# Kernel optimization log

Measured on AMD Instinct MI355X. Metric: run time of the kernel, lower is better.

Reference implementation:

```python
import jax, jax.numpy as jnp
import numpy as np

# dims: batch, seq(tokens, excl cls), input_dim, embed_dim, heads, ffn, experts, proto experts, classes
B, S, DIN, D, H, FF, E, P, NC = 2, 2048, 1024, 512, 8, 2048, 6, 4, 2
CAP = int(1.0 * S / E)  # capacity_factor=1.0


def _ln(x, g, b, eps=1e-5):
    m = x.mean(-1, keepdims=True)
    v = ((x - m) ** 2).mean(-1, keepdims=True)
    return (x - m) / jnp.sqrt(v + eps) * g + b


def _gelu(x):
    return jax.nn.gelu(x, approximate=False)


def _mha(x, in_w, in_b, out_w, out_b):
    # torch nn.MultiheadAttention, batch_first, eval (no dropout)
    b, s, d = x.shape
    dh = d // H
    qkv = x @ in_w.T + in_b
    q, k, v = jnp.split(qkv, 3, axis=-1)
    q = q.reshape(b, s, H, dh)
    k = k.reshape(b, s, H, dh)
    v = v.reshape(b, s, H, dh)
    att = jnp.einsum('bqhd,bkhd->bhqk', q, k) * (1.0 / np.sqrt(dh))
    att = jax.nn.softmax(att, axis=-1)
    o = jnp.einsum('bhqk,bkhd->bqhd', att, v).reshape(b, s, d)
    return o @ out_w.T + out_b


def _subln_ffn(x, w1, b1, lg, lb, w2, b2):
    # FeedForwardNetwork with subln: fc1 -> gelu -> LayerNorm -> fc2 (eval: no dropout)
    h = _gelu(x @ w1 + b1)
    h = _ln(h, lg, lb)
    return h @ w2 + b2


def _pamoe(x, gate_w, W1, b1, W2, b2):
    # top-1 prototype-augmented MoE with capacity-based token drop
    gate = jax.nn.softmax(x @ gate_w, axis=-1)          # [B,S,E]
    idx = jnp.argmax(gate, axis=-1)                      # [B,S]
    top_p = jnp.max(gate, axis=-1)                       # [B,S]
    oh = jax.nn.one_hot(idx, E, dtype=x.dtype)           # [B,S,E]
    pos = jnp.cumsum(oh, axis=1) * oh                    # position within expert
    keep = oh * (pos <= CAP)                             # capacity mask
    out = jnp.zeros_like(x)
    for e in range(E):  # small fixed loop over experts
        m = (keep[..., e] * top_p)[..., None]
        out = out + m * (_gelu(x @ W1[e] + b1[e]) @ W2[e] + b2[e])
    return out, gate


def _pamoe_ce(gate, labels):
    # CE between renormalized prototype-expert gate probs and cosine-sim labels
    p = gate[..., :P]
    logp = jnp.log(p / p.sum(-1, keepdims=True) + 1e-9)
    nll = -jnp.take_along_axis(logp, labels[..., None], axis=-1)[..., 0]
    return nll.mean()


def setup_inputs() -> dict:
    key = jax.random.key(0)
    cnt = [0]
    def nk():
        cnt[0] += 1
        return jax.random.fold_in(key, cnt[0])
    def w(*shape):
        return jax.random.normal(nk(), shape, dtype=jnp.float32) * 0.02
    d = {}
    d['x'] = jax.random.normal(nk(), (B, S, DIN), dtype=jnp.float32)
    d['protos'] = jax.random.normal(nk(), (P, DIN), dtype=jnp.float32)
    d['cls_token'] = jax.random.normal(nk(), (1, 1, D), dtype=jnp.float32)
    d['fc1_w'] = w(DIN, D); d['fc1_b'] = jnp.zeros((D,), jnp.float32)
    for li in ('l0', 'l1'):
        d[li + '_attn_in_w'] = w(3 * D, D); d[li + '_attn_in_b'] = jnp.zeros((3 * D,), jnp.float32)
        d[li + '_attn_out_w'] = w(D, D); d[li + '_attn_out_b'] = jnp.zeros((D,), jnp.float32)
        d[li + '_n1_g'] = jnp.ones((D,), jnp.float32); d[li + '_n1_b'] = jnp.zeros((D,), jnp.float32)
        d[li + '_n2_g'] = jnp.ones((D,), jnp.float32); d[li + '_n2_b'] = jnp.zeros((D,), jnp.float32)
    # layer0: pamoe + cls_ffn
    d['l0_cls_w1'] = w(D, FF); d['l0_cls_b1'] = jnp.zeros((FF,), jnp.float32)
    d['l0_cls_ln_g'] = jnp.ones((FF,), jnp.float32); d['l0_cls_ln_b'] = jnp.zeros((FF,), jnp.float32)
    d['l0_cls_w2'] = w(FF, D); d['l0_cls_b2'] = jnp.zeros((D,), jnp.float32)
    d['l0_gate_w'] = w(D, E)
    d['l0_e_w1'] = w(E, D, FF); d['l0_e_b1'] = jnp.zeros((E, FF), jnp.float32)
    d['l0_e_w2'] = w(E, FF, D); d['l0_e_b2'] = jnp.zeros((E, D), jnp.float32)
    # layer1: dense ffn
    d['l1_ffn_w1'] = w(D, FF); d['l1_ffn_b1'] = jnp.zeros((FF,), jnp.float32)
    d['l1_ffn_ln_g'] = jnp.ones((FF,), jnp.float32); d['l1_ffn_ln_b'] = jnp.zeros((FF,), jnp.float32)
    d['l1_ffn_w2'] = w(FF, D); d['l1_ffn_b2'] = jnp.zeros((D,), jnp.float32)
    d['norm_g'] = jnp.ones((D,), jnp.float32); d['norm_b'] = jnp.zeros((D,), jnp.float32)
    d['fc2_w'] = w(D, NC); d['fc2_b'] = jnp.zeros((NC,), jnp.float32)
    return d


def reference(x, protos, cls_token, fc1_w, fc1_b,
              l0_attn_in_w, l0_attn_in_b, l0_attn_out_w, l0_attn_out_b,
              l0_n1_g, l0_n1_b, l0_n2_g, l0_n2_b,
              l0_cls_w1, l0_cls_b1, l0_cls_ln_g, l0_cls_ln_b, l0_cls_w2, l0_cls_b2,
              l0_gate_w, l0_e_w1, l0_e_b1, l0_e_w2, l0_e_b2,
              l1_attn_in_w, l1_attn_in_b, l1_attn_out_w, l1_attn_out_b,
              l1_n1_g, l1_n1_b, l1_n2_g, l1_n2_b,
              l1_ffn_w1, l1_ffn_b1, l1_ffn_ln_g, l1_ffn_ln_b, l1_ffn_w2, l1_ffn_b2,
              norm_g, norm_b, fc2_w, fc2_b):
    # prototype cosine similarity on raw (detached) features -> routing supervision labels
    xr = jax.lax.stop_gradient(x)
    xn = xr / (jnp.linalg.norm(xr, axis=-1, keepdims=True) + 1e-8)
    pn = protos / (jnp.linalg.norm(protos, axis=-1, keepdims=True) + 1e-8)
    sim = jnp.einsum('bsd,pd->bsp', xn, pn)             # [B,S,P]
    labels = jnp.argmax(sim, axis=-1)                    # [B,S]

    h = x @ fc1_w + fc1_b                                # [B,S,D]
    cls = jnp.broadcast_to(cls_token, (h.shape[0], 1, D))
    h = jnp.concatenate([cls, h], axis=1)                # [B,S+1,D]

    # ---- layer 0 (pamoe block) ----
    attn = _mha(h, l0_attn_in_w, l0_attn_in_b, l0_attn_out_w, l0_attn_out_b)
    h = _ln(h, l0_n1_g, l0_n1_b)
    h = h + attn
    h = _ln(h, l0_n2_g, l0_n2_b)
    h_res = h
    c = _subln_ffn(h[:, 0:1], l0_cls_w1, l0_cls_b1, l0_cls_ln_g, l0_cls_ln_b, l0_cls_w2, l0_cls_b2)
    t, gate = _pamoe(h[:, 1:], l0_gate_w, l0_e_w1, l0_e_b1, l0_e_w2, l0_e_b2)
    h = h_res + jnp.concatenate([c, t], axis=1)          # pamoe residual
    loss_pamoe = _pamoe_ce(gate, labels)

    # ---- layer 1 (dense ffn block) ----
    attn = _mha(h, l1_attn_in_w, l1_attn_in_b, l1_attn_out_w, l1_attn_out_b)
    h = _ln(h, l1_n1_g, l1_n1_b)
    h = h + attn
    h = _ln(h, l1_n2_g, l1_n2_b)
    h = h + _subln_ffn(h, l1_ffn_w1, l1_ffn_b1, l1_ffn_ln_g, l1_ffn_ln_b, l1_ffn_w2, l1_ffn_b2)

    pooled = _ln(h, norm_g, norm_b)[:, 0]                # cls token
    logits = pooled @ fc2_w + fc2_b                      # [B,NC]
    return gate, logits, loss_pamoe
```

## Files before the change

kernel.cpp:

```cpp
#include <hip/hip_runtime.h>
#include <cmath>

#define DEVINL __device__ __forceinline__

typedef unsigned short ushort_t;
typedef unsigned int uint_t;

constexpr int Bb   = 2;
constexpr int Ss   = 2048;
constexpr int S1   = 2049;
constexpr int DIN  = 1024;
constexpr int Dd   = 512;
constexpr int Hh   = 8;
constexpr int FF   = 2048;
constexpr int Ee   = 6;
constexpr int NCc  = 2;
constexpr int CAP  = 341;
constexpr int NTOK = Bb * Ss;
constexpr int RR   = Bb * S1;
constexpr int MOE_ROWS = Bb * CAP;

typedef __attribute__((ext_vector_type(4))) float f32x4;
typedef __attribute__((ext_vector_type(8))) short bf16x8;

DEVINL float geluf(float x) { return 0.5f * x * (1.0f + erff(x * 0.7071067811865476f)); }

DEVINL ushort_t f2bf(float f) {
  uint_t u = __float_as_uint(f);
  u += 0x7FFFu + ((u >> 16) & 1u);
  return (ushort_t)(u >> 16);
}
DEVINL float bf2f(ushort_t u) { return __uint_as_float((uint_t)u << 16); }

DEVINL void glds16(const ushort_t* g, void* lds) {
  __builtin_amdgcn_global_load_lds(
      (const __attribute__((address_space(1))) void*)g,
      (__attribute__((address_space(3))) void*)lds, 16, 0, 0);
}

DEVINL float wsum(float v) {
#pragma unroll
  for (int off = 32; off; off >>= 1) v += __shfl_xor(v, off);
  return v;
}
DEVINL float bsum(float v, float* red) {
  v = wsum(v);
  int w = threadIdx.x >> 6;
  if ((threadIdx.x & 63) == 0) red[w] = v;
  __syncthreads();
  float r = red[0] + red[1] + red[2] + red[3];
  __syncthreads();
  return r;
}

constexpr int C5_N0 = NTOK * DIN / 8;
constexpr int C5_N1 = 3 * Dd * Dd / 8;
constexpr int C5_N2 = Dd * Dd / 8;
constexpr int C5_T  = C5_N0 + 2 * C5_N1 + 2 * C5_N2;
__global__ __launch_bounds__(256) void cast5_kernel(const float* __restrict__ s0, ushort_t* __restrict__ d0,
                                                    const float* __restrict__ s1, ushort_t* __restrict__ d1,
                                                    const float* __restrict__ s2, ushort_t* __restrict__ d2,
                                                    const float* __restrict__ s3, ushort_t* __restrict__ d3,
                                                    const float* __restrict__ s4, ushort_t* __restrict__ d4) {
  int i = blockIdx.x * 256 + threadIdx.x;
  if (i >= C5_T) return;
  const float* src; ushort_t* dst; int off;
  if (i < C5_N0) { src = s0; dst = d0; off = i; }
  else if (i < C5_N0 + C5_N1) { src = s1; dst = d1; off = i - C5_N0; }
  else if (i < C5_N0 + C5_N1 + C5_N2) { src = s2; dst = d2; off = i - C5_N0 - C5_N1; }
  else if (i < C5_N0 + 2 * C5_N1 + C5_N2) { src = s3; dst = d3; off = i - C5_N0 - C5_N1 - C5_N2; }
  else { src = s4; dst = d4; off = i - C5_N0 - 2 * C5_N1 - C5_N2; }
  float4 a = *(const float4*)(src + (size_t)off * 8);
  float4 b = *(const float4*)(src + (size_t)off * 8 + 4);
  bf16x8 v;
  v[0] = (short)f2bf(a.x); v[1] = (short)f2bf(a.y);
  v[2] = (short)f2bf(a.z); v[3] = (short)f2bf(a.w);
  v[4] = (short)f2bf(b.x); v[5] = (short)f2bf(b.y);
  v[6] = (short)f2bf(b.z); v[7] = (short)f2bf(b.w);
  *(bf16x8*)(dst + (size_t)off * 8) = v;
}

__global__ __launch_bounds__(256) void tpose_cast_kernel(const float* __restrict__ in,
                                                         ushort_t* __restrict__ outp,
                                                         int K, int N) {
  __shared__ float t[64][65];
  const int z = blockIdx.z;
  const float* src = in + (size_t)z * K * N;
  ushort_t* dst = outp + (size_t)z * K * N;
  const int k0 = blockIdx.x * 64, n0 = blockIdx.y * 64;
  const int tx = threadIdx.x & 15, ty = threadIdx.x >> 4;
#pragma unroll
  for (int p = 0; p < 4; ++p) {
    int k = ty + p * 16;
    float4 v = *(const float4*)(src + (size_t)(k0 + k) * N + n0 + tx * 4);
    t[k][tx * 4 + 0] = v.x; t[k][tx * 4 + 1] = v.y;
    t[k][tx * 4 + 2] = v.z; t[k][tx * 4 + 3] = v.w;
  }
  __syncthreads();
#pragma unroll
  for (int p = 0; p < 4; ++p) {
    int n = ty + p * 16;
    uint_t lo = (uint_t)f2bf(t[tx * 4 + 0][n]) | ((uint_t)f2bf(t[tx * 4 + 1][n]) << 16);
    uint_t hi = (uint_t)f2bf(t[tx * 4 + 2][n]) | ((uint_t)f2bf(t[tx * 4 + 3][n]) << 16);
    *(uint2*)(dst + (size_t)(n0 + n) * K + k0 + tx * 4) = make_uint2(lo, hi);
  }
}

__global__ __launch_bounds__(256) void labels_kernel(const float* __restrict__ x,
                                                     const float* __restrict__ protos,
                                                     int* __restrict__ lbl) {
  int t = blockIdx.x * 4 + (threadIdx.x >> 6);
  int lane = threadIdx.x & 63;
  if (t >= NTOK) return;
  const float* xr = x + (size_t)t * DIN;
  float xv[16];
  float ss = 0.f;
#pragma unroll
  for (int i = 0; i < 16; ++i) { xv[i] = xr[lane + 64 * i]; ss += xv[i] * xv[i]; }
  ss = wsum(ss);
  float nx = sqrtf(ss) + 1e-8f;
  float best = -2e30f; int bi = 0;
  for (int p = 0; p < 4; ++p) {
    const float* pr = protos + (size_t)p * DIN;
    float dp = 0.f, pp = 0.f;
#pragma unroll
    for (int i = 0; i < 16; ++i) { float v = pr[lane + 64 * i]; dp += v * xv[i]; pp += v * v; }
    dp = wsum(dp); pp = wsum(pp);
    float sim = dp / (nx * (sqrtf(pp) + 1e-8f));
    if (sim > best) { best = sim; bi = p; }
  }
  if (lane == 0) lbl[t] = bi;
}

template <bool ACT, bool SHIFT, int BMT>
__global__ __launch_bounds__(256) void mgemm_kernel(const ushort_t* __restrict__ A, int lda,
                                                    const ushort_t* __restrict__ Bw, int ldb,
                                                    const float* __restrict__ bias,
                                                    const ushort_t* __restrict__ res,
                                                    ushort_t* __restrict__ C, int ldc,
                                                    int M, int N, int K) {
  constexpr int MI = BMT / 32;
  __shared__ ushort_t As[BMT * 64];
  __shared__ ushort_t Bs[128 * 64];
  const int tid = threadIdx.x;
  const int l = tid & 63, l15 = l & 15, lg = l >> 4;
  const int w = tid >> 6;
  const int wm = w >> 1, wn = w & 1;
  const int bm = blockIdx.x * BMT, bn = blockIdx.y * 128;
  const int srowA = w * (BMT / 4) + (l >> 3);
  const int srowB = w * 32 + (l >> 3);
  const int scc = ((l & 7) ^ (l >> 3)) * 8;

  f32x4 acc[MI][4];
#pragma unroll
  for (int i = 0; i < MI; ++i)
#pragma unroll
    for (int j = 0; j < 4; ++j) acc[i][j] = (f32x4){0.f, 0.f, 0.f, 0.f};

  const ushort_t* agp[MI];
  const ushort_t* bgp[4];
#pragma unroll
  for (int j = 0; j < MI; ++j) {
    int ar = bm + srowA + j * 8; if (ar > M - 1) ar = M - 1;
    agp[j] = A + (size_t)ar * lda + scc;
  }
#pragma unroll
  for (int j = 0; j < 4; ++j)
    bgp[j] = Bw + (size_t)(bn + srowB + j * 8) * ldb + scc;

  for (int k0 = 0; k0 < K; k0 += 64) {
#pragma unroll
    for (int j = 0; j < MI; ++j)
      glds16(agp[j] + k0, (char*)As + w * (BMT * 32) + j * 1024);
#pragma unroll
    for (int j = 0; j < 4; ++j)
      glds16(bgp[j] + k0, (char*)Bs + w * 4096 + j * 1024);
    __syncthreads();
#pragma unroll
    for (int kc = 0; kc < 2; ++kc) {
      bf16x8 af[MI], bfr[4];
#pragma unroll
      for (int mi = 0; mi < MI; ++mi) {
        int row = wm * (BMT / 2) + mi * 16 + l15;
        af[mi] = *(const bf16x8*)((const char*)As +
                   ((row * 128 + (kc * 32 + lg * 8) * 2) ^ ((row & 7) << 4)));
      }
#pragma unroll
      for (int ni = 0; ni < 4; ++ni) {
        int row = wn * 64 + ni * 16 + l15;
        bfr[ni] = *(const bf16x8*)((const char*)Bs +
                   ((row * 128 + (kc * 32 + lg * 8) * 2) ^ ((row & 7) << 4)));
      }
#pragma unroll
      for (int mi = 0; mi < MI; ++mi)
#pragma unroll
        for (int ni = 0; ni < 4; ++ni)
          acc[mi][ni] = __builtin_amdgcn_mfma_f32_16x16x32_bf16(af[mi], bfr[ni], acc[mi][ni], 0, 0, 0);
    }
    __syncthreads();
  }

#pragma unroll
  for (int mi = 0; mi < MI; ++mi)
#pragma unroll
    for (int r = 0; r < 4; ++r) {
      int row = bm + wm * (BMT / 2) + mi * 16 + lg * 4 + r;
      if (row < M) {
        int orow = SHIFT ? (row + (row >> 11) + 1) : row;
#pragma unroll
        for (int ni = 0; ni < 4; ++ni) {
          int col = bn + wn * 64 + ni * 16 + l15;
          float t = acc[mi][ni][r];
          if (bias) t += bias[col];
          if (ACT) t = geluf(t);
          if (res) t += bf2f(res[(size_t)orow * ldc + col]);
          C[(size_t)orow * ldc + col] = f2bf(t);
        }
      }
    }
}

__global__ __launch_bounds__(256) void moe_mgemm1_kernel(const ushort_t* __restrict__ h2,
                                                         const ushort_t* __restrict__ w1T,
                                                         const float* __restrict__ b1all,
                                                         const int* __restrict__ list,
                                                         const int* __restrict__ cnt,
                                                         ushort_t* __restrict__ hid) {
  __shared__ ushort_t As[128 * 64];
  __shared__ ushort_t Bs[128 * 64];
  const int e = blockIdx.z;
  const int c0 = cnt[e * 2 + 0], c1 = cnt[e * 2 + 1];
  const ushort_t* Bw = w1T + (size_t)e * Dd * FF;
  const int tid = threadIdx.x;
  const int l = tid & 63, l15 = l & 15, lg = l >> 4;
  const int w = tid >> 6;
  const int wm = w >> 1, wn = w & 1;
  const int bm = blockIdx.x * 128, bn = blockIdx.y * 128;
  const int srow = w * 32 + (l >> 3);
  const int scc = ((l & 7) ^ (l >> 3)) * 8;

  f32x4 acc[4][4];
#pragma unroll
  for (int i = 0; i < 4; ++i)
#pragma unroll
    for (int j = 0; j < 4; ++j) acc[i][j] = (f32x4){0.f, 0.f, 0.f, 0.f};

  const ushort_t* agp[4];
  const ushort_t* bgp[4];
#pragma unroll
  for (int j = 0; j < 4; ++j) {
    int r = bm + srow + j * 8; if (r > MOE_ROWS - 1) r = MOE_ROWS - 1;
    int tok = list[e * MOE_ROWS + r] & (NTOK - 1);
    int b = tok >> 11, s = tok & (Ss - 1);
    agp[j] = h2 + (size_t)(b * S1 + s + 1) * Dd + scc;
    bgp[j] = Bw + (size_t)(bn + srow + j * 8) * Dd + scc;
  }

  for (int k0 = 0; k0 < Dd; k0 += 64) {
#pragma unroll
    for (int j = 0; j < 4; ++j) {
      glds16(agp[j] + k0, (char*)As + w * 4096 + j * 1024);
      glds16(bgp[j] + k0, (char*)Bs + w * 4096 + j * 1024);
    }
    __syncthreads();
#pragma unroll
    for (int kc = 0; kc < 2; ++kc) {
      bf16x8 af[4], bfr[4];
#pragma unroll
      for (int mi = 0; mi < 4; ++mi) {
        int row = wm * 64 + mi * 16 + l15;
        af[mi] = *(const bf16x8*)((const char*)As +
                   ((row * 128 + (kc * 32 + lg * 8) * 2) ^ ((row & 7) << 4)));
      }
#pragma unroll
      for (int ni = 0; ni < 4; ++ni) {
        int row = wn * 64 + ni * 16 + l15;
        bfr[ni] = *(const bf16x8*)((const char*)Bs +
                   ((row * 128 + (kc * 32 + lg * 8) * 2) ^ ((row & 7) << 4)));
      }
#pragma unroll
      for (int mi = 0; mi < 4; ++mi)
#pragma unroll
        for (int ni = 0; ni < 4; ++ni)
          acc[mi][ni] = __builtin_amdgcn_mfma_f32_16x16x32_bf16(af[mi], bfr[ni], acc[mi][ni], 0, 0, 0);
    }
    __syncthreads();
  }

#pragma unroll
  for (int mi = 0; mi < 4; ++mi)
#pragma unroll
    for (int rr = 0; rr < 4; ++rr) {
      int row = bm + wm * 64 + mi * 16 + lg * 4 + rr;
      bool v2 = (row < MOE_ROWS) && ((row < CAP) ? (row < c0) : ((row - CAP) < c1));
      if (v2) {
#pragma unroll
        for (int ni = 0; ni < 4; ++ni) {
          int col = bn + wn * 64 + ni * 16 + l15;
          hid[((size_t)e * MOE_ROWS + row) * FF + col] =
              f2bf(geluf(acc[mi][ni][rr] + b1all[e * FF + col]));
        }
      }
    }
}

template <int BMT>
__global__ __launch_bounds__(256) void moe_mgemm2_kernel(const ushort_t* __restrict__ hid,
                                                         const ushort_t* __restrict__ w2T,
                                                         const float* __restrict__ b2all,
                                                         const int* __restrict__ list,
                                                         const int* __restrict__ cnt,
                                                         const float* __restrict__ topp,
                                                         ushort_t* __restrict__ out) {
  constexpr int MI = BMT / 32;
  __shared__ ushort_t As[BMT * 64];
  __shared__ ushort_t Bs[128 * 64];
  const int e = blockIdx.z;
  const int c0 = cnt[e * 2 + 0], c1 = cnt[e * 2 + 1];
  const ushort_t* Bw = w2T + (size_t)e * FF * Dd;
  const int tid = threadIdx.x;
  const int l = tid & 63, l15 = l & 15, lg = l >> 4;
  const int w = tid >> 6;
  const int wm = w >> 1, wn = w & 1;
  const int bm = blockIdx.x * BMT, bn = blockIdx.y * 128;
  const int srowA = w * (BMT / 4) + (l >> 3);
  const int srowB = w * 32 + (l >> 3);
  const int scc = ((l & 7) ^ (l >> 3)) * 8;

  f32x4 acc[MI][4];
#pragma unroll
  for (int i = 0; i < MI; ++i)
#pragma unroll
    for (int j = 0; j < 4; ++j) acc[i][j] = (f32x4){0.f, 0.f, 0.f, 0.f};

  const ushort_t* agp[MI];
  const ushort_t* bgp[4];
#pragma unroll
  for (int j = 0; j < MI; ++j) {
    int r = bm + srowA + j * 8; if (r > MOE_ROWS - 1) r = MOE_ROWS - 1;
    agp[j] = hid + ((size_t)e * MOE_ROWS + r) * FF + scc;
  }
#pragma unroll
  for (int j = 0; j < 4; ++j)
    bgp[j] = Bw + (size_t)(bn + srowB + j * 8) * FF + scc;

  for (int k0 = 0; k0 < FF; k0 += 64) {
#pragma unroll
    for (int j = 0; j < MI; ++j)
      glds16(agp[j] + k0, (char*)As + w * (BMT * 32) + j * 1024);
#pragma unroll
    for (int j = 0; j < 4; ++j)
      glds16(bgp[j] + k0, (char*)Bs + w * 4096 + j * 1024);
    __syncthreads();
#pragma unroll
    for (int kc = 0; kc < 2; ++kc) {
      bf16x8 af[MI], bfr[4];
#pragma unroll
      for (int mi = 0; mi < MI; ++mi) {
        int row = wm * (BMT / 2) + mi * 16 + l15;
        af[mi] = *(const bf16x8*)((const char*)As +
                   ((row * 128 + (kc * 32 + lg * 8) * 2) ^ ((row & 7) << 4)));
      }
#pragma unroll
      for (int ni = 0; ni < 4; ++ni) {
        int row = wn * 64 + ni * 16 + l15;
        bfr[ni] = *(const bf16x8*)((const char*)Bs +
                   ((row * 128 + (kc * 32 + lg * 8) * 2) ^ ((row & 7) << 4)));
      }
#pragma unroll
      for (int mi = 0; mi < MI; ++mi)
#pragma unroll
        for (int ni = 0; ni < 4; ++ni)
          acc[mi][ni] = __builtin_amdgcn_mfma_f32_16x16x32_bf16(af[mi], bfr[ni], acc[mi][ni], 0, 0, 0);
    }
    __syncthreads();
  }

#pragma unroll
  for (int mi = 0; mi < MI; ++mi)
#pragma unroll
    for (int rr = 0; rr < 4; ++rr) {
      int row = bm + wm * (BMT / 2) + mi * 16 + lg * 4 + rr;
      bool v2 = (row < MOE_ROWS) && ((row < CAP) ? (row < c0) : ((row - CAP) < c1));
      if (v2) {
        int tok = list[e * MOE_ROWS + row];
        int b = tok >> 11, s = tok & (Ss - 1);
        float tp = topp[tok];
#pragma unroll
        for (int ni = 0; ni < 4; ++ni) {
          int col = bn + wn * 64 + ni * 16 + l15;
          size_t oidx = (size_t)(b * S1 + s + 1) * Dd + col;
          out[oidx] = f2bf(bf2f(out[oidx]) + tp * (acc[mi][ni][rr] + b2all[e * Dd + col]));
        }
      }
    }
}

__global__ __launch_bounds__(256) void cls_fill_kernel(const float* __restrict__ cls,
                                                       ushort_t* __restrict__ h) {
  int i = threadIdx.x;
  uint_t pk = (uint_t)f2bf(cls[i * 2]) | ((uint_t)f2bf(cls[i * 2 + 1]) << 16);
  *(uint_t*)(h + i * 2) = pk;
  *(uint_t*)(h + (size_t)S1 * Dd + i * 2) = pk;
}

template <int EPL>
__global__ __launch_bounds__(256) void ln_wave_kernel(const ushort_t* __restrict__ in,
                                                      const ushort_t* __restrict__ addv,
                                                      const float* __restrict__ g,
                                                      const float* __restrict__ bvec,
                                                      ushort_t* __restrict__ out,
                                                      ushort_t* __restrict__ out2,
                                                      int nrows) {
  constexpr int N = 64 * EPL;
  const int row = blockIdx.x * 4 + (threadIdx.x >> 6);
  const int lane = threadIdx.x & 63;
  if (row >= nrows) return;
  const size_t base = (size_t)row * N + lane * EPL;
  float xf[EPL];
  float s1 = 0.f, s2 = 0.f;
#pragma unroll
  for (int c = 0; c < EPL / 8; ++c) {
    bf16x8 x8 = *(const bf16x8*)(in + base + c * 8);
#pragma unroll
    for (int j = 0; j < 8; ++j) {
      float v = bf2f((ushort_t)x8[j]);
      xf[c * 8 + j] = v;
      s1 += v; s2 += v * v;
    }
  }
  s1 = wsum(s1); s2 = wsum(s2);
  float mean = s1 * (1.0f / N);
  float var = s2 * (1.0f / N) - mean * mean;
  float rstd = rsqrtf(var + 1e-5f);
#pragma unroll
  for (int c = 0; c < EPL / 8; ++c) {
    bf16x8 a8;
    if (addv) a8 = *(const bf16x8*)(addv + base + c * 8);
    bf16x8 o8;
#pragma unroll
    for (int j = 0; j < 8; ++j) {
      int col = lane * EPL + c * 8 + j;
      float v = (xf[c * 8 + j] - mean) * rstd * g[col] + bvec[col];
      if (addv) v += bf2f((ushort_t)a8[j]);
      o8[j] = (short)f2bf(v);
    }
    *(bf16x8*)(out + base + c * 8) = o8;
    if (out2) *(bf16x8*)(out2 + base + c * 8) = o8;
  }
}

__global__ __launch_bounds__(256) void ln2_wave_kernel(const ushort_t* __restrict__ in,
                                                       const ushort_t* __restrict__ addv,
                                                       const float* __restrict__ g1,
                                                       const float* __restrict__ b1,
                                                       const float* __restrict__ g2,
                                                       const float* __restrict__ b2,
                                                       ushort_t* __restrict__ out,
                                                       ushort_t* __restrict__ out2,
                                                       int nrows) {
  constexpr int N = 512;
  const int row = blockIdx.x * 4 + (threadIdx.x >> 6);
  const int lane = threadIdx.x & 63;
  if (row >= nrows) return;
  const size_t base = (size_t)row * N + lane * 8;
  bf16x8 x8 = *(const bf16x8*)(in + base);
  bf16x8 a8 = *(const bf16x8*)(addv + base);
  float xf[8];
  float s1 = 0.f, s2 = 0.f;
#pragma unroll
  for (int j = 0; j < 8; ++j) {
    float v = bf2f((ushort_t)x8[j]);
    xf[j] = v; s1 += v; s2 += v * v;
  }
  s1 = wsum(s1); s2 = wsum(s2);
  float mean = s1 * (1.0f / N);
  float rstd = rsqrtf(s2 * (1.0f / N) - mean * mean + 1e-5f);
  float vf[8];
  float t1 = 0.f, t2 = 0.f;
#pragma unroll
  for (int j = 0; j < 8; ++j) {
    int col = lane * 8 + j;
    float v = (xf[j] - mean) * rstd * g1[col] + b1[col] + bf2f((ushort_t)a8[j]);
    vf[j] = v; t1 += v; t2 += v * v;
  }
  t1 = wsum(t1); t2 = wsum(t2);
  float mean2 = t1 * (1.0f / N);
  float rstd2 = rsqrtf(t2 * (1.0f / N) - mean2 * mean2 + 1e-5f);
  bf16x8 o8;
#pragma unroll
  for (int j = 0; j < 8; ++j) {
    int col = lane * 8 + j;
    o8[j] = (short)f2bf((vf[j] - mean2) * rstd2 * g2[col] + b2[col]);
  }
  *(bf16x8*)(out + base) = o8;
  if (out2) *(bf16x8*)(out2 + base) = o8;
}

__global__ __launch_bounds__(256) void attn_mfma_kernel(const ushort_t* __restrict__ qkv,
                                                        ushort_t* __restrict__ o) {
  __shared__ ushort_t Ksh[128 * 64];
  __shared__ ushort_t Vt[64 * 128];
  const int tid = threadIdx.x;
  const int w = tid >> 6, l = tid & 63;
  const int l15 = l & 15, lg = l >> 4;
  const int hh = blockIdx.y, b = blockIdx.z;
  const int qblk = blockIdx.x * 64;
  const size_t rbase = (size_t)b * S1 * 1536;
  const float CEXP = 0.125f * 1.4426950408889634f;

  bf16x8 aq[2];
  {
    int qr = qblk + w * 16 + l15;
    const ushort_t* qp = qkv + rbase + (size_t)qr * 1536 + hh * 64;
#pragma unroll
    for (int dc = 0; dc < 2; ++dc)
      aq[dc] = (qr < S1) ? *(const bf16x8*)(qp + dc * 32 + lg * 8)
                         : (bf16x8){0, 0, 0, 0, 0, 0, 0, 0};
  }

  f32x4 ovac[4];
#pragma unroll
  for (int dt = 0; dt < 4; ++dt) ovac[dt] = (f32x4){0.f, 0.f, 0.f, 0.f};
  float m_r = -1e30f, l_r = 0.f;

  const int kcc = ((l & 7) ^ (l >> 3)) * 8;
  const int krloc = w * 32 + (l >> 3);
  const int sv_k0 = (tid & 63) * 2, sv_d0 = (tid >> 6) * 16;

  for (int it = 0; it < 17; ++it) {
    {
      int rb = it * 128 + krloc;
#pragma unroll
      for (int pass = 0; pass < 4; ++pass) {
        int key = rb + pass * 8;
        if (key > S1 - 1) key = S1 - 1;
        glds16(qkv + rbase + (size_t)key * 1536 + 512 + hh * 64 + kcc,
               (char*)Ksh + w * 4096 + pass * 1024);
      }
    }
    {
      int key0 = it * 128 + sv_k0;
      int k0c = (key0 > S1 - 1) ? S1 - 1 : key0;
      int k1c = (key0 + 1 > S1 - 1) ? S1 - 1 : key0 + 1;
      const ushort_t* vp0 = qkv + rbase + (size_t)k0c * 1536 + 1024 + hh * 64 + sv_d0;
      const ushort_t* vp1 = qkv + rbase + (size_t)k1c * 1536 + 1024 + hh * 64 + sv_d0;
      bf16x8 va0 = *(const bf16x8*)(vp0), va1 = *(const bf16x8*)(vp0 + 8);
      bf16x8 vb0 = *(const bf16x8*)(vp1), vb1 = *(const bf16x8*)(vp1 + 8);
#pragma unroll
      for (int i = 0; i < 8; ++i) {
        int d0 = sv_d0 + i, d1 = sv_d0 + 8 + i;
        uint_t p0 = (uint_t)(ushort_t)va0[i] | ((uint_t)(ushort_t)vb0[i] << 16);
        uint_t p1 = (uint_t)(ushort_t)va1[i] | ((uint_t)(ushort_t)vb1[i] << 16);
        *(uint_t*)((char*)Vt + ((d0 * 256 + sv_k0 * 2) ^ ((d0 & 7) << 4))) = p0;
        *(uint_t*)((char*)Vt + ((d1 * 256 + sv_k0 * 2) ^ ((d1 & 7) << 4))) = p1;
      }
    }
    __syncthreads();

    f32x4 s[8];
    __builtin_amdgcn_s_setprio(1);
#pragma unroll
    for (int kt = 0; kt < 8; ++kt) {
      f32x4 acc = (f32x4){0.f, 0.f, 0.f, 0.f};
      const int krow = kt * 16 + l15;
      const int rswz = (krow & 7) << 4;
#pragma unroll
      for (int dc = 0; dc < 2; ++dc) {
        bf16x8 kb = *(const bf16x8*)((const char*)Ksh + (((krow * 64 + dc * 32 + lg * 8) * 2) ^ rswz));
        acc = __builtin_amdgcn_mfma_f32_16x16x32_bf16(kb, aq[dc], acc, 0, 0, 0);
      }
      s[kt] = acc;
    }
    __builtin_amdgcn_s_setprio(0);
    if (it == 16) {
#pragma unroll
      for (int kt = 0; kt < 8; ++kt)
#pragma unroll
        for (int r = 0; r < 4; ++r)
          if (2048 + kt * 16 + lg * 4 + r >= S1) s[kt][r] = -1e30f;
    }

    f32x4 m4 = s[0];
#pragma unroll
    for (int kt = 1; kt < 8; ++kt)
#pragma unroll
      for (int r = 0; r < 4; ++r) m4[r] = fmaxf(m4[r], s[kt][r]);
    float mx = fmaxf(fmaxf(m4[0], m4[1]), fmaxf(m4[2], m4[3]));
    mx = fmaxf(mx, __shfl_xor(mx, 16));
    mx = fmaxf(mx, __shfl_xor(mx, 32));
    if (!__all(mx <= m_r + 8.0f)) {
      float mn = fmaxf(m_r, mx);
      float fac = __builtin_amdgcn_exp2f((m_r - mn) * CEXP);
      m_r = mn;
      float facq[4];
#pragma unroll
      for (int r = 0; r < 4; ++r) facq[r] = __shfl(fac, lg * 4 + r);
#pragma unroll
      for (int dt = 0; dt < 4; ++dt)
#pragma unroll
        for (int r = 0; r < 4; ++r) ovac[dt][r] *= facq[r];
      l_r *= fac;
    }
    float mc = m_r * CEXP;
    float rs = 0.f;
#pragma unroll
    for (int kt = 0; kt < 8; ++kt)
#pragma unroll
      for (int r = 0; r < 4; ++r) {
        float pv = __builtin_amdgcn_exp2f(s[kt][r] * CEXP - mc);
        s[kt][r] = pv;
        rs += pv;
      }
    rs += __shfl_xor(rs, 16);
    rs += __shfl_xor(rs, 32);
    l_r += rs;

    uint_t pk[8][2];
#pragma unroll
    for (int kt = 0; kt < 8; ++kt) {
      pk[kt][0] = (uint_t)f2bf(s[kt][0]) | ((uint_t)f2bf(s[kt][1]) << 16);
      pk[kt][1] = (uint_t)f2bf(s[kt][2]) | ((uint_t)f2bf(s[kt][3]) << 16);
    }

    bf16x8 pa[4];
#pragma unroll
    for (int kh = 0; kh < 4; ++kh) {
      union { uint_t u[4]; bf16x8 v; } cu;
#pragma unroll
      for (int wd = 0; wd < 4; ++wd) {
        int src = (((2 * lg + (wd >> 1)) & 3) << 4) + l15;
        uint_t c0 = (uint_t)__shfl((int)pk[kh * 2 + 0][wd & 1], src);
        uint_t c1 = (uint_t)__shfl((int)pk[kh * 2 + 1][wd & 1], src);
        cu.u[wd] = (lg & 2) ? c1 : c0;
      }
      pa[kh] = cu.v;
    }

    __builtin_amdgcn_s_setprio(1);
#pragma unroll
    for (int kh = 0; kh < 4; ++kh)
#pragma unroll
      for (int dt = 0; dt < 4; ++dt) {
        const int vrow = dt * 16 + l15;
        bf16x8 vb = *(const bf16x8*)((const char*)Vt +
                      (((vrow * 256 + (kh * 32 + lg * 8) * 2)) ^ ((vrow & 7) << 4)));
        ovac[dt] = __builtin_amdgcn_mfma_f32_16x16x32_bf16(pa[kh], vb, ovac[dt], 0, 0, 0);
      }
    __builtin_amdgcn_s_setprio(0);
    __syncthreads();
  }

  float invq[4];
#pragma unroll
  for (int r = 0; r < 4; ++r) invq[r] = 1.0f / __shfl(l_r, lg * 4 + r);
#pragma unroll
  for (int r = 0; r < 4; ++r) {
    int qq = qblk + w * 16 + lg * 4 + r;
    if (qq < S1) {
      ushort_t* orow = o + (size_t)(b * S1 + qq) * Dd + hh * 64;
#pragma unroll
      for (int dt = 0; dt < 4; ++dt) orow[dt * 16 + l15] = f2bf(ovac[dt][r] * invq[r]);
    }
  }
}

__global__ __launch_bounds__(256) void gate_kernel(const ushort_t* __restrict__ h2,
                                                   const float* __restrict__ gw,
                                                   float* __restrict__ gate_out,
                                                   float* __restrict__ topp,
                                                   int* __restrict__ idx) {
  int t = blockIdx.x * 4 + (threadIdx.x >> 6);
  int lane = threadIdx.x & 63;
  if (t >= NTOK) return;
  int b = t >> 11, s = t & (Ss - 1);
  const ushort_t* hr = h2 + (size_t)(b * S1 + s + 1) * Dd;
  bf16x8 h8 = *(const bf16x8*)(hr + lane * 8);
  float acc[6] = {};
#pragma unroll
  for (int j = 0; j < 8; ++j) {
    int d = lane * 8 + j;
    float xv = bf2f((ushort_t)h8[j]);
    const float* g = gw + (size_t)d * Ee;
#pragma unroll
    for (int e = 0; e < 6; ++e) acc[e] += xv * g[e];
  }
#pragma unroll
  for (int e = 0; e < 6; ++e) acc[e] = wsum(acc[e]);
  if (lane == 0) {
    float mx = acc[0];
#pragma unroll
    for (int e = 1; e < 6; ++e) mx = fmaxf(mx, acc[e]);
    float ex[6], sum = 0.f;
#pragma unroll
    for (int e = 0; e < 6; ++e) { ex[e] = __expf(acc[e] - mx); sum += ex[e]; }
    float invs = 1.0f / sum;
    int best = 0; float bp = ex[0];
#pragma unroll
    for (int e = 1; e < 6; ++e) { if (ex[e] > bp) { bp = ex[e]; best = e; } }
#pragma unroll
    for (int e = 0; e < 6; ++e) gate_out[(size_t)t * Ee + e] = ex[e] * invs;
    topp[t] = bp * invs;
    idx[t] = best;
  }
}

__global__ __launch_bounds__(256) void route_kernel(const int* __restrict__ idx,
                                                    int* __restrict__ list,
                                                    int* __restrict__ cnt) {
  __shared__ int cnts[256];
  __shared__ int tot;
  const int e = blockIdx.x, b = blockIdx.y;
  const int tid = threadIdx.x;
  const int s0 = tid * 8;
  int loc[8];
  int c = 0;
#pragma unroll
  for (int j = 0; j < 8; ++j) {
    int t = b * Ss + s0 + j;
    if (idx[t] == e) loc[c++] = t;
  }
  cnts[tid] = c;
  __syncthreads();
  if (tid == 0) {
    int run = 0;
    for (int i = 0; i < 256; ++i) { int v = cnts[i]; cnts[i] = run; run += v; }
    tot = run;
  }
  __syncthreads();
  int base = cnts[tid];
  for (int j = 0; j < c; ++j) {
    int pos = base + j;
    if (pos < CAP) list[e * MOE_ROWS + b * CAP + pos] = loc[j];
  }
  if (tid == 0) cnt[e * Bb + b] = (tot < CAP) ? tot : CAP;
}

__global__ __launch_bounds__(256) void cls_ffn1_kernel(const ushort_t* __restrict__ h2,
                                                       const float* __restrict__ w1,
                                                       const float* __restrict__ b1,
                                                       float* __restrict__ chid) {
  __shared__ float hrow[Dd];
  __shared__ float red[8][32];
  const int b = blockIdx.y, tid = threadIdx.x;
  const int cl = tid & 31, kp = tid >> 5;
  const int col = blockIdx.x * 32 + cl;
  const ushort_t* hr = h2 + (size_t)(b * S1) * Dd;
  hrow[tid] = bf2f(hr[tid]);
  hrow[tid + 256] = bf2f(hr[tid + 256]);
  __syncthreads();
  float acc = 0.f;
#pragma unroll 8
  for (int j = 0; j < 64; ++j) {
    int d = kp * 64 + j;
    acc += hrow[d] * w1[(size_t)d * FF + col];
  }
  red[kp][cl] = acc;
  __syncthreads();
  if (kp == 0) {
    float s = b1[col];
#pragma unroll
    for (int i = 0; i < 8; ++i) s += red[i][cl];
    chid[b * FF + col] = geluf(s);
  }
}

__global__ __launch_bounds__(256) void cls_ln_kernel(const float* __restrict__ chid,
                                                     const float* __restrict__ lg,
                                                     const float* __restrict__ lb,
                                                     float* __restrict__ chln) {
  __shared__ float red[8];
  const int b = blockIdx.x, tid = threadIdx.x;
  const float* hr = chid + b * FF;
  float hv[8];
  float s1 = 0.f, s2 = 0.f;
#pragma unroll
  for (int j = 0; j < 8; ++j) {
    hv[j] = hr[tid + j * 256];
    s1 += hv[j]; s2 += hv[j] * hv[j];
  }
  s1 = bsum(s1, red);
  s2 = bsum(s2, red);
  float mean = s1 * (1.0f / FF);
  float rstd = rsqrtf(s2 * (1.0f / FF) - mean * mean + 1e-5f);
#pragma unroll
  for (int j = 0; j < 8; ++j) {
    int k = tid + j * 256;
    chln[b * FF + k] = (hv[j] - mean) * rstd * lg[k] + lb[k];
  }
}

__global__ __launch_bounds__(256) void cls_ffn2_kernel(const float* __restrict__ chln,
                                                       const float* __restrict__ w2,
                                                       const float* __restrict__ b2,
                                                       ushort_t* __restrict__ outbuf) {
  __shared__ float red[8][32];
  const int b = blockIdx.y, tid = threadIdx.x;
  const int cl = tid & 31, kp = tid >> 5;
  const int col = blockIdx.x * 32 + cl;
  const float* hr = chln + b * FF;
  float acc = 0.f;
#pragma unroll 8
  for (int j = 0; j < 256; ++j) {
    int k = kp * 256 + j;
    acc += hr[k] * w2[(size_t)k * Dd + col];
  }
  red[kp][cl] = acc;
  __syncthreads();
  if (kp == 0) {
    float s = b2[col];
#pragma unroll
    for (int i = 0; i < 8; ++i) s += red[i][cl];
    size_t oidx = (size_t)(b * S1) * Dd + col;
    outbuf[oidx] = f2bf(bf2f(outbuf[oidx]) + s);
  }
}

__global__ __launch_bounds__(256) void loss_part_kernel(const float* __restrict__ gate,
                                                        const int* __restrict__ lbl,
                                                        float* __restrict__ part) {
  __shared__ float red[8];
  int t = blockIdx.x * 256 + threadIdx.x;
  float v = 0.f;
  if (t < NTOK) {
    const float* p = gate + (size_t)t * Ee;
    float sum = p[0] + p[1] + p[2] + p[3];
    float pl = p[lbl[t]];
    v = -logf(pl / sum + 1e-9f);
  }
  v = bsum(v, red);
  if (threadIdx.x == 0) part[blockIdx.x] = v;
}

__global__ void loss_final_kernel(const float* __restrict__ part, float* __restrict__ out) {
  if (threadIdx.x == 0) {
    float s = 0.f;
    for (int i = 0; i < 16; ++i) s += part[i];
    out[NTOK * Ee + Bb * NCc] = s / (float)NTOK;
  }
}

__global__ __launch_bounds__(256) void final_head_kernel(const ushort_t* __restrict__ h,
                                                         const float* __restrict__ g,
                                                         const float* __restrict__ bvec,
                                                         const float* __restrict__ w,
                                                         const float* __restrict__ fb,
                                                         float* __restrict__ out) {
  __shared__ float red[8];
  int b = blockIdx.x, tid = threadIdx.x;
  const ushort_t* hr = h + (size_t)(b * S1) * Dd;
  float x0 = bf2f(hr[tid]), x1 = bf2f(hr[tid + 256]);
  float s1 = bsum(x0 + x1, red);
  float s2 = bsum(x0 * x0 + x1 * x1, red);
  float mean = s1 * (1.0f / Dd);
  float var = s2 * (1.0f / Dd) - mean * mean;
  float rstd = rsqrtf(var + 1e-5f);
  float p0 = (x0 - mean) * rstd * g[tid] + bvec[tid];
  float p1 = (x1 - mean) * rstd * g[tid + 256] + bvec[tid + 256];
  float l0 = p0 * w[tid * 2 + 0] + p1 * w[(tid + 256) * 2 + 0];
  float l1 = p0 * w[tid * 2 + 1] + p1 * w[(tid + 256) * 2 + 1];
  l0 = bsum(l0, red);
  l1 = bsum(l1, red);
  if (tid == 0) {
    out[NTOK * Ee + b * NCc + 0] = l0 + fb[0];
    out[NTOK * Ee + b * NCc + 1] = l1 + fb[1];
  }
}

extern "C" void kernel_launch(void* const* d_in, const int* in_sizes, int n_in,
                              void* d_out, int out_size, void* d_ws, size_t ws_size,
                              hipStream_t stream) {
  (void)in_sizes; (void)n_in; (void)out_size; (void)ws_size;
  const float* x       = (const float*)d_in[0];
  const float* protos  = (const float*)d_in[1];
  const float* cls_tok = (const float*)d_in[2];
  const float* fc1_w   = (const float*)d_in[3];
  const float* fc1_b   = (const float*)d_in[4];
  const float* a0_in_w = (const float*)d_in[5];
  const float* a0_in_b = (const float*)d_in[6];
  const float* a0_out_w= (const float*)d_in[7];
  const float* a0_out_b= (const float*)d_in[8];
  const float* n1g0    = (const float*)d_in[9];
  const float* n1b0    = (const float*)d_in[10];
  const float* n2g0    = (const float*)d_in[11];
  const float* n2b0    = (const float*)d_in[12];
  const float* a1_in_w = (const float*)d_in[13];
  const float* a1_in_b = (const float*)d_in[14];
  const float* a1_out_w= (const float*)d_in[15];
  const float* a1_out_b= (const float*)d_in[16];
  const float* n1g1    = (const float*)d_in[17];
  const float* n1b1    = (const float*)d_in[18];
  const float* n2g1    = (const float*)d_in[19];
  const float* n2b1    = (const float*)d_in[20];
  const float* cw1     = (const float*)d_in[21];
  const float* cb1     = (const float*)d_in[22];
  const float* clg     = (const float*)d_in[23];
  const float* clb     = (const float*)d_in[24];
  const float* cw2     = (const float*)d_in[25];
  const float* cb2     = (const float*)d_in[26];
  const float* gate_w  = (const float*)d_in[27];
  const float* ew1     = (const float*)d_in[28];
  const float* eb1     = (const float*)d_in[29];
  const float* ew2     = (const float*)d_in[30];
  const float* eb2     = (const float*)d_in[31];
  const float* fw1     = (const float*)d_in[32];
  const float* fb1     = (const float*)d_in[33];
  const float* flg     = (const float*)d_in[34];
  const float* flb     = (const float*)d_in[35];
  const float* fw2     = (const float*)d_in[36];
  const float* fb2     = (const float*)d_in[37];
  const float* ng      = (const float*)d_in[38];
  const float* nb      = (const float*)d_in[39];
  const float* fc2_w   = (const float*)d_in[40];
  const float* fc2_b   = (const float*)d_in[41];
  float* out = (float*)d_out;

  char* base = (char*)d_ws;
  size_t o = 0;
  auto alloc = [&](size_t bytes) -> void* {
    void* p = base + o;
    o += (bytes + 255) & ~(size_t)255;
    return p;
  };
  ushort_t* UB0  = (ushort_t*)alloc((size_t)RR * Dd * 2);
  ushort_t* UB1  = (ushort_t*)alloc((size_t)RR * Dd * 2);
  ushort_t* UB2  = (ushort_t*)alloc((size_t)RR * Dd * 2);
  ushort_t* BIGU = (ushort_t*)alloc((size_t)RR * FF * 2);
  ushort_t* XB   = (ushort_t*)alloc((size_t)NTOK * DIN * 2);
  ushort_t* WQ0  = (ushort_t*)alloc((size_t)3 * Dd * Dd * 2);
  ushort_t* WO0  = (ushort_t*)alloc((size_t)Dd * Dd * 2);
  ushort_t* WQ1  = (ushort_t*)alloc((size_t)3 * Dd * Dd * 2);
  ushort_t* WO1  = (ushort_t*)alloc((size_t)Dd * Dd * 2);
  ushort_t* WF1T = (ushort_t*)alloc((size_t)Dd * DIN * 2);
  ushort_t* WE1T = (ushort_t*)alloc((size_t)Ee * FF * Dd * 2);
  ushort_t* WE2T = (ushort_t*)alloc((size_t)Ee * Dd * FF * 2);
  ushort_t* WFW1T= (ushort_t*)alloc((size_t)FF * Dd * 2);
  ushort_t* WFW2T= (ushort_t*)alloc((size_t)Dd * FF * 2);
  float* TOPP = (float*)alloc(NTOK * 4);
  float* PART = (float*)alloc(64 * 4);
  float* CHID = (float*)alloc(Bb * FF * 4);
  float* CHLN = (float*)alloc(Bb * FF * 4);
  int* LBL  = (int*)alloc(NTOK * 4);
  int* IDX  = (int*)alloc(NTOK * 4);
  int* LIST = (int*)alloc(Ee * MOE_ROWS * 4);
  int* CNT  = (int*)alloc(Ee * Bb * 4);

  const int ln_grid = (RR + 3) / 4;

  cast5_kernel<<<(C5_T + 255) / 256, 256, 0, stream>>>(
      x, XB, a0_in_w, WQ0, a0_out_w, WO0, a1_in_w, WQ1, a1_out_w, WO1);
  tpose_cast_kernel<<<dim3(DIN / 64, Dd / 64, 1), 256, 0, stream>>>(fc1_w, WF1T, DIN, Dd);
  tpose_cast_kernel<<<dim3(Dd / 64, FF / 64, Ee), 256, 0, stream>>>(ew1, WE1T, Dd, FF);
  tpose_cast_kernel<<<dim3(FF / 64, Dd / 64, Ee), 256, 0, stream>>>(ew2, WE2T, FF, Dd);
  tpose_cast_kernel<<<dim3(Dd / 64, FF / 64, 1), 256, 0, stream>>>(fw1, WFW1T, Dd, FF);
  tpose_cast_kernel<<<dim3(FF / 64, Dd / 64, 1), 256, 0, stream>>>(fw2, WFW2T, FF, Dd);

  labels_kernel<<<NTOK / 4, 256, 0, stream>>>(x, protos, LBL);
  mgemm_kernel<false, true, 64><<<dim3(64, 4), 256, 0, stream>>>(
      XB, DIN, WF1T, DIN, fc1_b, nullptr, UB0, Dd, NTOK, Dd, DIN);
  cls_fill_kernel<<<1, 256, 0, stream>>>(cls_tok, UB0);

  mgemm_kernel<false, false, 64><<<dim3(65, 12), 256, 0, stream>>>(
      UB0, Dd, WQ0, Dd, a0_in_b, nullptr, BIGU, 3 * Dd, RR, 3 * Dd, Dd);
  attn_mfma_kernel<<<dim3(33, Hh, Bb), 256, 0, stream>>>(BIGU, UB1);
  mgemm_kernel<false, false, 64><<<dim3(65, 4), 256, 0, stream>>>(
      UB1, Dd, WO0, Dd, a0_out_b, nullptr, UB2, Dd, RR, Dd, Dd);
  ln2_wave_kernel<<<ln_grid, 256, 0, stream>>>(UB0, UB2, n1g0, n1b0, n2g0, n2b0, UB0, UB2, RR);

  cls_ffn1_kernel<<<dim3(FF / 32, Bb), 256, 0, stream>>>(UB0, cw1, cb1, CHID);
  cls_ln_kernel<<<Bb, 256, 0, stream>>>(CHID, clg, clb, CHLN);
  cls_ffn2_kernel<<<dim3(Dd / 32, Bb), 256, 0, stream>>>(CHLN, cw2, cb2, UB2);
  gate_kernel<<<NTOK / 4, 256, 0, stream>>>(UB0, gate_w, out, TOPP, IDX);
  route_kernel<<<dim3(Ee, Bb), 256, 0, stream>>>(IDX, LIST, CNT);
  moe_mgemm1_kernel<<<dim3(6, 16, Ee), 256, 0, stream>>>(UB0, WE1T, eb1, LIST, CNT, BIGU);
  moe_mgemm2_kernel<64><<<dim3(11, 4, Ee), 256, 0, stream>>>(BIGU, WE2T, eb2, LIST, CNT, TOPP, UB2);
  loss_part_kernel<<<16, 256, 0, stream>>>(out, LBL, PART);
  loss_final_kernel<<<1, 64, 0, stream>>>(PART, out);

  mgemm_kernel<false, false, 64><<<dim3(65, 12), 256, 0, stream>>>(
      UB2, Dd, WQ1, Dd, a1_in_b, nullptr, BIGU, 3 * Dd, RR, 3 * Dd, Dd);
  attn_mfma_kernel<<<dim3(33, Hh, Bb), 256, 0, stream>>>(BIGU, UB1);
  mgemm_kernel<false, false, 64><<<dim3(65, 4), 256, 0, stream>>>(
      UB1, Dd, WO1, Dd, a1_out_b, nullptr, UB0, Dd, RR, Dd, Dd);
  ln2_wave_kernel<<<ln_grid, 256, 0, stream>>>(UB2, UB0, n1g1, n1b1, n2g1, n2b1, UB2, nullptr, RR);

  mgemm_kernel<true, false, 128><<<dim3(33, 16), 256, 0, stream>>>(
      UB2, Dd, WFW1T, Dd, fb1, nullptr, BIGU, FF, RR, FF, Dd);
  ln_wave_kernel<32><<<ln_grid, 256, 0, stream>>>(BIGU, nullptr, flg, flb, BIGU, nullptr, RR);
  mgemm_kernel<false, false, 64><<<dim3(65, 4), 256, 0, stream>>>(
      BIGU, FF, WFW2T, FF, fb2, UB2, UB0, Dd, RR, Dd, FF);

  final_head_kernel<<<Bb, 256, 0, stream>>>(UB0, ng, nb, fc2_w, fc2_b, out);
}
```

Measured before the change: 491.2 us.

## Double-buffer attention K/V loads, shrink MoE and FFN1 GEMM row tiles

The attention kernel now double-buffers the K tile in shared memory and prefetches the next block's V into registers while the current block computes. V is written transposed into a padded, re-swizzled layout after the compute step, which removes the load-then-sync stall at the top of each iteration. Separately, the MoE first GEMM is templated on row tile size and launched with 64-row tiles, and the dense FFN1 GEMM also switches to 64-row tiles. Both launch more blocks to fill the GPU better, at the cost of more weight reloads and extra LDS use and syncs in attention.

New measurement: 507.8 us. 1.03x slower.

```diff
diff --git a/kernel.cpp b/kernel.cpp
--- a/kernel.cpp
+++ b/kernel.cpp
@@ -220,13 +220,15 @@
     }
 }
 
+template <int BMT>
 __global__ __launch_bounds__(256) void moe_mgemm1_kernel(const ushort_t* __restrict__ h2,
                                                          const ushort_t* __restrict__ w1T,
                                                          const float* __restrict__ b1all,
                                                          const int* __restrict__ list,
                                                          const int* __restrict__ cnt,
                                                          ushort_t* __restrict__ hid) {
-  __shared__ ushort_t As[128 * 64];
+  constexpr int MI = BMT / 32;
+  __shared__ ushort_t As[BMT * 64];
   __shared__ ushort_t Bs[128 * 64];
   const int e = blockIdx.z;
   const int c0 = cnt[e * 2 + 0], c1 = cnt[e * 2 + 1];
@@ -235,40 +237,44 @@
   const int l = tid & 63, l15 = l & 15, lg = l >> 4;
   const int w = tid >> 6;
   const int wm = w >> 1, wn = w & 1;
-  const int bm = blockIdx.x * 128, bn = blockIdx.y * 128;
-  const int srow = w * 32 + (l >> 3);
+  const int bm = blockIdx.x * BMT, bn = blockIdx.y * 128;
+  const int srowA = w * (BMT / 4) + (l >> 3);
+  const int srowB = w * 32 + (l >> 3);
   const int scc = ((l & 7) ^ (l >> 3)) * 8;
 
-  f32x4 acc[4][4];
-#pragma unroll
-  for (int i = 0; i < 4; ++i)
+  f32x4 acc[MI][4];
+#pragma unroll
+  for (int i = 0; i < MI; ++i)
 #pragma unroll
     for (int j = 0; j < 4; ++j) acc[i][j] = (f32x4){0.f, 0.f, 0.f, 0.f};
 
-  const ushort_t* agp[4];
+  const ushort_t* agp[MI];
   const ushort_t* bgp[4];
 #pragma unroll
-  for (int j = 0; j < 4; ++j) {
-    int r = bm + srow + j * 8; if (r > MOE_ROWS - 1) r = MOE_ROWS - 1;
+  for (int j = 0; j < MI; ++j) {
+    int r = bm + srowA + j * 8; if (r > MOE_ROWS - 1) r = MOE_ROWS - 1;
     int tok = list[e * MOE_ROWS + r] & (NTOK - 1);
     int b = tok >> 11, s = tok & (Ss - 1);
     agp[j] = h2 + (size_t)(b * S1 + s + 1) * Dd + scc;
-    bgp[j] = Bw + (size_t)(bn + srow + j * 8) * Dd + scc;
-  }
+  }
+#pragma unroll
+  for (int j = 0; j < 4; ++j)
+    bgp[j] = Bw + (size_t)(bn + srowB + j * 8) * Dd + scc;
 
   for (int k0 = 0; k0 < Dd; k0 += 64) {
 #pragma unroll
-    for (int j = 0; j < 4; ++j) {
-      glds16(agp[j] + k0, (char*)As + w * 4096 + j * 1024);
+    for (int j = 0; j < MI; ++j)
+      glds16(agp[j] + k0, (char*)As + w * (BMT * 32) + j * 1024);
+#pragma unroll
+    for (int j = 0; j < 4; ++j)
       glds16(bgp[j] + k0, (char*)Bs + w * 4096 + j * 1024);
-    }
     __syncthreads();
 #pragma unroll
     for (int kc = 0; kc < 2; ++kc) {
-      bf16x8 af[4], bfr[4];
-#pragma unroll
-      for (int mi = 0; mi < 4; ++mi) {
-        int row = wm * 64 + mi * 16 + l15;
+      bf16x8 af[MI], bfr[4];
+#pragma unroll
+      for (int mi = 0; mi < MI; ++mi) {
+        int row = wm * (BMT / 2) + mi * 16 + l15;
         af[mi] = *(const bf16x8*)((const char*)As +
                    ((row * 128 + (kc * 32 + lg * 8) * 2) ^ ((row & 7) << 4)));
       }
@@ -279,7 +285,7 @@
                    ((row * 128 + (kc * 32 + lg * 8) * 2) ^ ((row & 7) << 4)));
       }
 #pragma unroll
-      for (int mi = 0; mi < 4; ++mi)
+      for (int mi = 0; mi < MI; ++mi)
 #pragma unroll
         for (int ni = 0; ni < 4; ++ni)
           acc[mi][ni] = __builtin_amdgcn_mfma_f32_16x16x32_bf16(af[mi], bfr[ni], acc[mi][ni], 0, 0, 0);
@@ -288,10 +294,10 @@
   }
 
 #pragma unroll
-  for (int mi = 0; mi < 4; ++mi)
+  for (int mi = 0; mi < MI; ++mi)
 #pragma unroll
     for (int rr = 0; rr < 4; ++rr) {
-      int row = bm + wm * 64 + mi * 16 + lg * 4 + rr;
+      int row = bm + wm * (BMT / 2) + mi * 16 + lg * 4 + rr;
       bool v2 = (row < MOE_ROWS) && ((row < CAP) ? (row < c0) : ((row - CAP) < c1));
       if (v2) {
 #pragma unroll
@@ -499,8 +505,8 @@
 
 __global__ __launch_bounds__(256) void attn_mfma_kernel(const ushort_t* __restrict__ qkv,
                                                         ushort_t* __restrict__ o) {
-  __shared__ ushort_t Ksh[128 * 64];
-  __shared__ ushort_t Vt[64 * 128];
+  __shared__ ushort_t Ksh[2][128 * 64];
+  __shared__ ushort_t Vt[64 * 136];
   const int tid = threadIdx.x;
   const int w = tid >> 6, l = tid & 63;
   const int l15 = l & 15, lg = l >> 4;
@@ -525,38 +531,44 @@
   float m_r = -1e30f, l_r = 0.f;
 
   const int kcc = ((l & 7) ^ (l >> 3)) * 8;
-  const int krloc = w * 32 + (l >> 3);
-  const int sv_k0 = (tid & 63) * 2, sv_d0 = (tid >> 6) * 16;
+  const int rloc = w * 32 + (l >> 3);
+  const int vd0 = (l & 7) * 8;
+
+  bf16x8 vreg[4];
+  {
+#pragma unroll
+    for (int p = 0; p < 4; ++p) {
+      int key = rloc + p * 8;
+      glds16(qkv + rbase + (size_t)key * 1536 + 512 + hh * 64 + kcc,
+             (char*)Ksh[0] + w * 4096 + p * 1024);
+      vreg[p] = *(const bf16x8*)(qkv + rbase + (size_t)key * 1536 + 1024 + hh * 64 + vd0);
+    }
+#pragma unroll
+    for (int p = 0; p < 4; ++p) {
+      int lk = rloc + p * 8;
+#pragma unroll
+      for (int j = 0; j < 8; ++j) {
+        int d = vd0 + j;
+        *(ushort_t*)((char*)Vt + (((d * 272 + lk * 2)) ^ (((d >> 3) & 7) << 4))) =
+            (ushort_t)vreg[p][j];
+      }
+    }
+    __syncthreads();
+  }
 
   for (int it = 0; it < 17; ++it) {
-    {
-      int rb = it * 128 + krloc;
-#pragma unroll
-      for (int pass = 0; pass < 4; ++pass) {
-        int key = rb + pass * 8;
+    const int cur = it & 1;
+    if (it < 16) {
+      int nb = (it + 1) * 128 + rloc;
+#pragma unroll
+      for (int p = 0; p < 4; ++p) {
+        int key = nb + p * 8;
         if (key > S1 - 1) key = S1 - 1;
         glds16(qkv + rbase + (size_t)key * 1536 + 512 + hh * 64 + kcc,
-               (char*)Ksh + w * 4096 + pass * 1024);
-      }
-    }
-    {
-      int key0 = it * 128 + sv_k0;
-      int k0c = (key0 > S1 - 1) ? S1 - 1 : key0;
-      int k1c = (key0 + 1 > S1 - 1) ? S1 - 1 : key0 + 1;
-      const ushort_t* vp0 = qkv + rbase + (size_t)k0c * 1536 + 1024 + hh * 64 + sv_d0;
-      const ushort_t* vp1 = qkv + rbase + (size_t)k1c * 1536 + 1024 + hh * 64 + sv_d0;
-      bf16x8 va0 = *(const bf16x8*)(vp0), va1 = *(const bf16x8*)(vp0 + 8);
-      bf16x8 vb0 = *(const bf16x8*)(vp1), vb1 = *(const bf16x8*)(vp1 + 8);
-#pragma unroll
-      for (int i = 0; i < 8; ++i) {
-        int d0 = sv_d0 + i, d1 = sv_d0 + 8 + i;
-        uint_t p0 = (uint_t)(ushort_t)va0[i] | ((uint_t)(ushort_t)vb0[i] << 16);
-        uint_t p1 = (uint_t)(ushort_t)va1[i] | ((uint_t)(ushort_t)vb1[i] << 16);
-        *(uint_t*)((char*)Vt + ((d0 * 256 + sv_k0 * 2) ^ ((d0 & 7) << 4))) = p0;
-        *(uint_t*)((char*)Vt + ((d1 * 256 + sv_k0 * 2) ^ ((d1 & 7) << 4))) = p1;
-      }
-    }
-    __syncthreads();
+               (char*)Ksh[cur ^ 1] + w * 4096 + p * 1024);
+        vreg[p] = *(const bf16x8*)(qkv + rbase + (size_t)key * 1536 + 1024 + hh * 64 + vd0);
+      }
+    }
 
     f32x4 s[8];
     __builtin_amdgcn_s_setprio(1);
@@ -567,7 +579,8 @@
       const int rswz = (krow & 7) << 4;
 #pragma unroll
       for (int dc = 0; dc < 2; ++dc) {
-        bf16x8 kb = *(const bf16x8*)((const char*)Ksh + (((krow * 64 + dc * 32 + lg * 8) * 2) ^ rswz));
+        bf16x8 kb = *(const bf16x8*)((const char*)Ksh[cur] +
+                     (((krow * 64 + dc * 32 + lg * 8) * 2) ^ rswz));
         acc = __builtin_amdgcn_mfma_f32_16x16x32_bf16(kb, aq[dc], acc, 0, 0, 0);
       }
       s[kt] = acc;
@@ -644,11 +657,25 @@
       for (int dt = 0; dt < 4; ++dt) {
         const int vrow = dt * 16 + l15;
         bf16x8 vb = *(const bf16x8*)((const char*)Vt +
-                      (((vrow * 256 + (kh * 32 + lg * 8) * 2)) ^ ((vrow & 7) << 4)));
+                      (((vrow * 272 + (kh * 32 + lg * 8) * 2)) ^ (((vrow >> 3) & 7) << 4)));
         ovac[dt] = __builtin_amdgcn_mfma_f32_16x16x32_bf16(pa[kh], vb, ovac[dt], 0, 0, 0);
       }
     __builtin_amdgcn_s_setprio(0);
     __syncthreads();
+
+    if (it < 16) {
+#pragma unroll
+      for (int p = 0; p < 4; ++p) {
+        int lk = rloc + p * 8;
+#pragma unroll
+        for (int j = 0; j < 8; ++j) {
+          int d = vd0 + j;
+          *(ushort_t*)((char*)Vt + (((d * 272 + lk * 2)) ^ (((d >> 3) & 7) << 4))) =
+              (ushort_t)vreg[p][j];
+        }
+      }
+      __syncthreads();
+    }
   }
 
   float invq[4];
@@ -972,7 +999,7 @@
   cls_ffn2_kernel<<<dim3(Dd / 32, Bb), 256, 0, stream>>>(CHLN, cw2, cb2, UB2);
   gate_kernel<<<NTOK / 4, 256, 0, stream>>>(UB0, gate_w, out, TOPP, IDX);
   route_kernel<<<dim3(Ee, Bb), 256, 0, stream>>>(IDX, LIST, CNT);
-  moe_mgemm1_kernel<<<dim3(6, 16, Ee), 256, 0, stream>>>(UB0, WE1T, eb1, LIST, CNT, BIGU);
+  moe_mgemm1_kernel<64><<<dim3(11, 16, Ee), 256, 0, stream>>>(UB0, WE1T, eb1, LIST, CNT, BIGU);
   moe_mgemm2_kernel<64><<<dim3(11, 4, Ee), 256, 0, stream>>>(BIGU, WE2T, eb2, LIST, CNT, TOPP, UB2);
   loss_part_kernel<<<16, 256, 0, stream>>>(out, LBL, PART);
   loss_final_kernel<<<1, 64, 0, stream>>>(PART, out);
@@ -984,7 +1011,7 @@
       UB1, Dd, WO1, Dd, a1_out_b, nullptr, UB0, Dd, RR, Dd, Dd);
   ln2_wave_kernel<<<ln_grid, 256, 0, stream>>>(UB2, UB0, n1g1, n1b1, n2g1, n2b1, UB2, nullptr, RR);
 
-  mgemm_kernel<true, false, 128><<<dim3(33, 16), 256, 0, stream>>>(
+  mgemm_kernel<true, false, 64><<<dim3(65, 16), 256, 0, stream>>>(
       UB2, Dd, WFW1T, Dd, fb1, nullptr, BIGU, FF, RR, FF, Dd);
   ln_wave_kernel<32><<<ln_grid, 256, 0, stream>>>(BIGU, nullptr, flg, flb, BIGU, nullptr, RR);
   mgemm_kernel<false, false, 64><<<dim3(65, 4), 256, 0, stream>>>(
```
